# Optimization experiments

Measured on AMD Instinct MI355X. Metric: run time of the kernel, lower is better.

## Reference

```python
import jax, jax.numpy as jnp
import numpy as np

B, OUT, IN = 1024, 512, 1024

def setup_inputs() -> dict:
    key = jax.random.key(0)
    k1, k2, k3, k4 = jax.random.split(key, 4)
    x = jax.random.uniform(k1, (B, IN), dtype=jnp.float32)            # inputs in [0,1]
    w = jax.random.uniform(k2, (OUT, IN), dtype=jnp.float32)          # centers in [min_input, max_input]=[0,1]
    u = jax.random.uniform(k3, (OUT, IN), dtype=jnp.float32, minval=0.2, maxval=0.7)  # slopes per init
    andor01 = jax.random.randint(k4, (1, OUT), 0, 2).astype(jnp.float32)  # frozen 0/1 mix ('*' mode)
    return {"x": x, "w": w, "u": u, "andor01": andor01}

def reference(x, w, u, andor01):
    # xuw = u * (x[b,None,i] - w[o,i]) ; z[b,o] = sum_i xuw^2 ; y = exp(-z)
    diff = u[None, :, :] * (x[:, None, :] - w[None, :, :])   # [B, OUT, IN]
    z = jnp.sum(diff * diff, axis=-1)                        # [B, OUT]
    y = jnp.exp(-z)                                          # forward of LargeAttractorExp
    # andor == '*': y + andor01 * (1 - 2y)
    return y + andor01 * (1.0 - 2.0 * y)
```

## Files before the change

### kernel.cpp

```cpp
#include <hip/hip_runtime.h>

#define B_SZ   1024
#define OUT_SZ 512
#define IN_SZ  1024

#define MB 64
#define NB 32
#define NKC 16

typedef __bf16 bf16x8 __attribute__((ext_vector_type(8)));
typedef __bf16 bf16x4 __attribute__((ext_vector_type(4)));
typedef float  f32x4  __attribute__((ext_vector_type(4)));

#define A_IDX(seg, s, mf, slot) (((((seg)*2 + (s))*4 + (mf))*64 + (slot))*8)
#define B_IDX(seg, s, nf, slot) (((((seg)*2 + (s))*2 + (nf))*64 + (slot))*8)

__global__ __launch_bounds__(512) void rbf_one(
    const float* __restrict__ x, const float* __restrict__ w,
    const float* __restrict__ u, const float* __restrict__ andor,
    float* __restrict__ out)
{
    __shared__ __bf16 Asm[2 * 2 * 4 * 64 * 8];
    __shared__ __bf16 Bsm[2 * 2 * 2 * 64 * 8];
    __shared__ float  r_lds[NB];

    const int t    = threadIdx.x;
    const int lane = t & 63;
    const int wv   = t >> 6;
    const int wm   = wv >> 1;
    const int wn   = wv & 1;

    const int bid = blockIdx.x;
    const int swz = (bid & 7) * 32 + (bid >> 3);
    const int mT = swz & 15, nT = swz >> 4;
    const int mBase = mT * MB, nBase = nT * NB;

    f32x4 acc = {};
    float rp = 0.f;

    const int arow = t >> 4;
    const int akl  = (t & 15) * 4;
    const int brow = t >> 4;

    float4 xr[2], ur, wr;
    auto load_regs = [&](int c) {
        const int gk = c * 64 + akl;
        xr[0] = *(const float4*)&x[(size_t)(mBase + arow)      * IN_SZ + gk];
        xr[1] = *(const float4*)&x[(size_t)(mBase + 32 + arow) * IN_SZ + gk];
        ur    = *(const float4*)&u[(size_t)(nBase + brow)      * IN_SZ + gk];
        wr    = *(const float4*)&w[(size_t)(nBase + brow)      * IN_SZ + gk];
    };

    const int sW   = akl >> 5;
    const int quad = (akl >> 3) & 3;
    const int j0   = akl & 7;

    auto write_lds = [&]() {
        #pragma unroll
        for (int i = 0; i < 2; ++i) {
            const int row   = i * 32 + arow;
            const int frag  = row >> 4;
            const int slot  = quad * 16 + (((row & 15) ^ quad) & 15);
            float v[4] = {xr[i].x, xr[i].y, xr[i].z, xr[i].w};
            bf16x4 a0, a1;
            #pragma unroll
            for (int e = 0; e < 4; ++e) {
                a0[e] = (__bf16)(v[e] * v[e]);
                a1[e] = (__bf16)v[e];
            }
            *(bf16x4*)&Asm[A_IDX(0, sW, frag, slot) + j0] = a0;
            *(bf16x4*)&Asm[A_IDX(1, sW, frag, slot) + j0] = a1;
        }
        {
            const int frag = brow >> 4;
            const int slot = quad * 16 + (((brow & 15) ^ quad) & 15);
            float uv[4] = {ur.x, ur.y, ur.z, ur.w};
            float wv4[4] = {wr.x, wr.y, wr.z, wr.w};
            bf16x4 b0, b1;
            #pragma unroll
            for (int e = 0; e < 4; ++e) {
                float u2 = uv[e] * uv[e];
                float p  = uv[e] * wv4[e];
                b0[e] = (__bf16)u2;
                b1[e] = (__bf16)(-2.f * u2 * wv4[e]);
                rp = fmaf(p, p, rp);
            }
            *(bf16x4*)&Bsm[B_IDX(0, sW, frag, slot) + j0] = b0;
            *(bf16x4*)&Bsm[B_IDX(1, sW, frag, slot) + j0] = b1;
        }
    };

    const int r_quad = lane >> 4;
    const int r_slot = r_quad * 16 + (((lane & 15) ^ r_quad) & 15);

    load_regs(0);
    for (int c = 0; c < NKC; ++c) {
        __syncthreads();
        write_lds();
        __syncthreads();
        if (c + 1 < NKC) load_regs(c + 1);
        #pragma unroll
        for (int seg = 0; seg < 2; ++seg)
            #pragma unroll
            for (int s2 = 0; s2 < 2; ++s2) {
                bf16x8 am = *(const bf16x8*)&Asm[A_IDX(seg, s2, wm, r_slot)];
                bf16x8 bn = *(const bf16x8*)&Bsm[B_IDX(seg, s2, wn, r_slot)];
                acc = __builtin_amdgcn_mfma_f32_16x16x32_bf16(am, bn, acc, 0, 0, 0);
            }
    }

    rp += __shfl_xor(rp, 1);
    rp += __shfl_xor(rp, 2);
    rp += __shfl_xor(rp, 4);
    rp += __shfl_xor(rp, 8);
    if ((lane & 15) == 0) r_lds[brow] = rp;
    __syncthreads();

    const int col = lane & 15, rq = lane >> 4;
    const int b = mBase + wm * 16 + rq * 4;
    const int o = nBase + wn * 16 + col;
    const float rv = r_lds[wn * 16 + col];
    const float a  = andor[o];
    const float cf = 1.f - 2.f * a;
    #pragma unroll
    for (int r = 0; r < 4; ++r) {
        float y = __expf(-(acc[r] + rv));
        out[(size_t)(b + r) * OUT_SZ + o] = fmaf(y, cf, a);
    }
}

extern "C" void kernel_launch(void* const* d_in, const int* in_sizes, int n_in,
                              void* d_out, int out_size, void* d_ws, size_t ws_size,
                              hipStream_t stream) {
    const float* x = (const float*)d_in[0];
    const float* w = (const float*)d_in[1];
    const float* u = (const float*)d_in[2];
    const float* a = (const float*)d_in[3];
    float* out = (float*)d_out;

    rbf_one<<<dim3((B_SZ / MB) * (OUT_SZ / NB)), dim3(512), 0, stream>>>(
        x, w, u, a, out);
}
```

Before: 75.87 us.

## Shrink M tile, double K chunk, and split K across wave pairs

Halves the batch tile to 32 rows, doubling the grid to 512 blocks, and processes 128-wide K chunks, which halves the number of barrier-separated iterations. The eight waves now form a 2x2 output grid times 2 K-halves, and the two K-halves are reduced through shared memory before the epilogue. Loading and transform work is balanced so every thread handles x, u and w. The aim is more blocks in flight for occupancy and less per-chunk synchronisation. In exchange, the u/w tile is transformed twice as often across blocks, and the kernel adds a cross-wave reduction and an extra barrier.

```diff
diff --git a/kernel.cpp b/kernel.cpp
--- a/kernel.cpp
+++ b/kernel.cpp
@@ -4,87 +4,82 @@
 #define OUT_SZ 512
 #define IN_SZ  1024
 
-#define MB 64
+#define MB 32
 #define NB 32
-#define NKC 16
+#define CH 128
+#define NKC (IN_SZ / CH)
 
 typedef __bf16 bf16x8 __attribute__((ext_vector_type(8)));
 typedef __bf16 bf16x4 __attribute__((ext_vector_type(4)));
 typedef float  f32x4  __attribute__((ext_vector_type(4)));
 
-#define A_IDX(seg, s, mf, slot) (((((seg)*2 + (s))*4 + (mf))*64 + (slot))*8)
-#define B_IDX(seg, s, nf, slot) (((((seg)*2 + (s))*2 + (nf))*64 + (slot))*8)
+#define A_IDX(seg, s, f, slot) (((((seg)*4 + (s))*2 + (f))*64 + (slot))*8)
+#define B_IDX(seg, s, f, slot) (((((seg)*4 + (s))*2 + (f))*64 + (slot))*8)
 
-__global__ __launch_bounds__(512) void rbf_one(
+__global__ __launch_bounds__(512, 4) void rbf_one(
     const float* __restrict__ x, const float* __restrict__ w,
     const float* __restrict__ u, const float* __restrict__ andor,
     float* __restrict__ out)
 {
-    __shared__ __bf16 Asm[2 * 2 * 4 * 64 * 8];
-    __shared__ __bf16 Bsm[2 * 2 * 2 * 64 * 8];
+    __shared__ __bf16 Asm[2 * 4 * 2 * 64 * 8];
+    __shared__ __bf16 Bsm[2 * 4 * 2 * 64 * 8];
+    __shared__ float  accsm[4 * 64 * 4];
     __shared__ float  r_lds[NB];
 
     const int t    = threadIdx.x;
     const int lane = t & 63;
     const int wv   = t >> 6;
-    const int wm   = wv >> 1;
-    const int wn   = wv & 1;
+    const int ks   = wv & 1;
+    const int wn   = (wv >> 1) & 1;
+    const int wm   = (wv >> 2) & 1;
 
     const int bid = blockIdx.x;
-    const int swz = (bid & 7) * 32 + (bid >> 3);
-    const int mT = swz & 15, nT = swz >> 4;
+    const int swz = (bid & 7) * 64 + (bid >> 3);
+    const int nT = swz >> 5, mT = swz & 31;
     const int mBase = mT * MB, nBase = nT * NB;
 
     f32x4 acc = {};
     float rp = 0.f;
 
-    const int arow = t >> 4;
-    const int akl  = (t & 15) * 4;
-    const int brow = t >> 4;
+    const int row = t >> 4;
+    const int k4  = (t & 15) * 4;
 
-    float4 xr[2], ur, wr;
+    float4 xr[2], ur[2], wr[2];
     auto load_regs = [&](int c) {
-        const int gk = c * 64 + akl;
-        xr[0] = *(const float4*)&x[(size_t)(mBase + arow)      * IN_SZ + gk];
-        xr[1] = *(const float4*)&x[(size_t)(mBase + 32 + arow) * IN_SZ + gk];
-        ur    = *(const float4*)&u[(size_t)(nBase + brow)      * IN_SZ + gk];
-        wr    = *(const float4*)&w[(size_t)(nBase + brow)      * IN_SZ + gk];
+        #pragma unroll
+        for (int h = 0; h < 2; ++h) {
+            const int gk = c * CH + h * 64 + k4;
+            xr[h] = *(const float4*)&x[(size_t)(mBase + row) * IN_SZ + gk];
+            ur[h] = *(const float4*)&u[(size_t)(nBase + row) * IN_SZ + gk];
+            wr[h] = *(const float4*)&w[(size_t)(nBase + row) * IN_SZ + gk];
+        }
     };
-
-    const int sW   = akl >> 5;
-    const int quad = (akl >> 3) & 3;
-    const int j0   = akl & 7;
 
     auto write_lds = [&]() {
         #pragma unroll
-        for (int i = 0; i < 2; ++i) {
-            const int row   = i * 32 + arow;
-            const int frag  = row >> 4;
-            const int slot  = quad * 16 + (((row & 15) ^ quad) & 15);
-            float v[4] = {xr[i].x, xr[i].y, xr[i].z, xr[i].w};
-            bf16x4 a0, a1;
+        for (int h = 0; h < 2; ++h) {
+            const int kl   = h * 64 + k4;
+            const int sW   = kl >> 5;
+            const int quad = (kl >> 3) & 3;
+            const int j0   = kl & 7;
+            const int frag = row >> 4;
+            const int slot = quad * 16 + (((row & 15) ^ quad) & 15);
+            float xv[4]  = {xr[h].x, xr[h].y, xr[h].z, xr[h].w};
+            float uv[4]  = {ur[h].x, ur[h].y, ur[h].z, ur[h].w};
+            float wv4[4] = {wr[h].x, wr[h].y, wr[h].z, wr[h].w};
+            bf16x4 a0, a1, b0, b1;
             #pragma unroll
             for (int e = 0; e < 4; ++e) {
-                a0[e] = (__bf16)(v[e] * v[e]);
-                a1[e] = (__bf16)v[e];
+                float xe = xv[e], ue = uv[e], we = wv4[e];
+                float u2 = ue * ue, p = ue * we;
+                a0[e] = (__bf16)(xe * xe);
+                a1[e] = (__bf16)xe;
+                b0[e] = (__bf16)u2;
+                b1[e] = (__bf16)(-2.f * u2 * we);
+                rp = fmaf(p, p, rp);
             }
             *(bf16x4*)&Asm[A_IDX(0, sW, frag, slot) + j0] = a0;
             *(bf16x4*)&Asm[A_IDX(1, sW, frag, slot) + j0] = a1;
-        }
-        {
-            const int frag = brow >> 4;
-            const int slot = quad * 16 + (((brow & 15) ^ quad) & 15);
-            float uv[4] = {ur.x, ur.y, ur.z, ur.w};
-            float wv4[4] = {wr.x, wr.y, wr.z, wr.w};
-            bf16x4 b0, b1;
-            #pragma unroll
-            for (int e = 0; e < 4; ++e) {
-                float u2 = uv[e] * uv[e];
-                float p  = uv[e] * wv4[e];
-                b0[e] = (__bf16)u2;
-                b1[e] = (__bf16)(-2.f * u2 * wv4[e]);
-                rp = fmaf(p, p, rp);
-            }
             *(bf16x4*)&Bsm[B_IDX(0, sW, frag, slot) + j0] = b0;
             *(bf16x4*)&Bsm[B_IDX(1, sW, frag, slot) + j0] = b1;
         }
@@ -95,16 +90,16 @@
 
     load_regs(0);
     for (int c = 0; c < NKC; ++c) {
-        __syncthreads();
+        if (c) __syncthreads();
         write_lds();
         __syncthreads();
         if (c + 1 < NKC) load_regs(c + 1);
         #pragma unroll
         for (int seg = 0; seg < 2; ++seg)
             #pragma unroll
-            for (int s2 = 0; s2 < 2; ++s2) {
-                bf16x8 am = *(const bf16x8*)&Asm[A_IDX(seg, s2, wm, r_slot)];
-                bf16x8 bn = *(const bf16x8*)&Bsm[B_IDX(seg, s2, wn, r_slot)];
+            for (int sh = 0; sh < 2; ++sh) {
+                bf16x8 am = *(const bf16x8*)&Asm[A_IDX(seg, ks * 2 + sh, wm, r_slot)];
+                bf16x8 bn = *(const bf16x8*)&Bsm[B_IDX(seg, ks * 2 + sh, wn, r_slot)];
                 acc = __builtin_amdgcn_mfma_f32_16x16x32_bf16(am, bn, acc, 0, 0, 0);
             }
     }
@@ -113,19 +108,26 @@
     rp += __shfl_xor(rp, 2);
     rp += __shfl_xor(rp, 4);
     rp += __shfl_xor(rp, 8);
-    if ((lane & 15) == 0) r_lds[brow] = rp;
+    if ((lane & 15) == 0) r_lds[row] = rp;
+
+    __syncthreads();
+    if (ks == 1)
+        *(f32x4*)&accsm[((wm * 2 + wn) * 64 + lane) * 4] = acc;
     __syncthreads();
 
-    const int col = lane & 15, rq = lane >> 4;
-    const int b = mBase + wm * 16 + rq * 4;
-    const int o = nBase + wn * 16 + col;
-    const float rv = r_lds[wn * 16 + col];
-    const float a  = andor[o];
-    const float cf = 1.f - 2.f * a;
-    #pragma unroll
-    for (int r = 0; r < 4; ++r) {
-        float y = __expf(-(acc[r] + rv));
-        out[(size_t)(b + r) * OUT_SZ + o] = fmaf(y, cf, a);
+    if (ks == 0) {
+        f32x4 o4 = *(const f32x4*)&accsm[((wm * 2 + wn) * 64 + lane) * 4];
+        const int col = lane & 15, rq = lane >> 4;
+        const int b = mBase + wm * 16 + rq * 4;
+        const int o = nBase + wn * 16 + col;
+        const float rv = r_lds[wn * 16 + col];
+        const float a  = andor[o];
+        const float cf = 1.f - 2.f * a;
+        #pragma unroll
+        for (int r = 0; r < 4; ++r) {
+            float y = __expf(-(acc[r] + o4[r] + rv));
+            out[(size_t)(b + r) * OUT_SZ + o] = fmaf(y, cf, a);
+        }
     }
 }
 
```

New measurement: 73.40 us. 3.2% less time.
